# Performance work log

Hardware: AMD Instinct MI355X
Metric: run time of the kernel (lower is better)

Reference implementation:

```python
import jax, jax.numpy as jnp
import numpy as np

N_NODES = 100000
N_EDGES = 600000
N_GRAPHS = 512
VOCAB = 4096
EMB = 128
HID = 128


def setup_inputs() -> dict:
    key = jax.random.key(0)
    ks = jax.random.split(key, 8)
    x = jax.random.randint(ks[0], (N_NODES,), 0, VOCAB)
    edge_index = jax.random.randint(ks[1], (2, N_EDGES), 0, N_NODES)
    batch = jnp.sort(jax.random.randint(ks[2], (N_NODES,), 0, N_GRAPHS))
    emb = jax.random.normal(ks[3], (VOCAB, EMB), dtype=jnp.float32)
    W1 = jax.random.normal(ks[4], (EMB, HID), dtype=jnp.float32) / np.sqrt(EMB)
    b1 = jnp.zeros((HID,), dtype=jnp.float32)
    W2 = jax.random.normal(ks[5], (HID, HID), dtype=jnp.float32) / np.sqrt(HID)
    b2 = jnp.zeros((HID,), dtype=jnp.float32)
    return {"x": x, "edge_index": edge_index, "batch": batch,
            "emb": emb, "W1": W1, "b1": b1, "W2": W2, "b2": b2}


def gcn_conv(h, src, dst, W, b, n_nodes):
    # PyG GCNConv: linear transform, then symmetric-normalized scatter-sum
    # (self-loops already included in src/dst), plus bias.
    h = h @ W
    deg = jax.ops.segment_sum(jnp.ones(dst.shape, h.dtype), dst, num_segments=n_nodes)
    dis = jnp.where(deg > 0, jax.lax.rsqrt(jnp.maximum(deg, 1.0)), 0.0)
    norm = dis[src] * dis[dst]                      # [E]
    msg = h[src] * norm[:, None]                    # gather + scale
    out = jax.ops.segment_sum(msg, dst, num_segments=n_nodes)
    return out + b


def reference(x, edge_index, batch, emb, W1, b1, W2, b2):
    n = x.shape[0]
    loop = jnp.arange(n)
    src = jnp.concatenate([edge_index[0], loop])    # add self-loops, as GCNConv does
    dst = jnp.concatenate([edge_index[1], loop])

    h = emb[x]                                      # [N, EMB] embedding lookup
    h = jax.nn.relu(gcn_conv(h, src, dst, W1, b1, n))
    # dropout: identity in eval mode
    h = gcn_conv(h, src, dst, W2, b2, n)            # [N, HID]

    # global_mean_pool over graph ids
    sums = jax.ops.segment_sum(h, batch, num_segments=N_GRAPHS)
    cnts = jax.ops.segment_sum(jnp.ones((n,), h.dtype), batch, num_segments=N_GRAPHS)
    return sums / jnp.maximum(cnts, 1.0)[:, None]   # [N_GRAPHS, HID]
```

## Files before the change

### kernel.cpp

```cpp
#include <hip/hip_runtime.h>
#include <hip/hip_bf16.h>
#include <hip/hip_fp16.h>

#define D 128

__device__ __forceinline__ float bf2f(unsigned short u) {
  return __uint_as_float(((unsigned int)u) << 16);
}
__device__ __forceinline__ unsigned short f2bf(float f) {
  unsigned int x = __float_as_uint(f);
  x += 0x7fff + ((x >> 16) & 1);
  return (unsigned short)(x >> 16);
}
__device__ __forceinline__ float h2f(unsigned short b) {
  return __half2float(__ushort_as_half(b));
}
__device__ __forceinline__ float2 up2(unsigned int u) {
  __half2 h = *reinterpret_cast<__half2*>(&u);
  return __half22float2(h);
}
__device__ __forceinline__ void fma8h(float* a, uint4 v, float w) {
  float2 t;
  t = up2(v.x); a[0] += w * t.x; a[1] += w * t.y;
  t = up2(v.y); a[2] += w * t.x; a[3] += w * t.y;
  t = up2(v.z); a[4] += w * t.x; a[5] += w * t.y;
  t = up2(v.w); a[6] += w * t.x; a[7] += w * t.y;
}
__device__ __forceinline__ void add8(float* a, uint4 v) {
  a[0] += __uint_as_float(v.x << 16);
  a[1] += __uint_as_float(v.x & 0xffff0000u);
  a[2] += __uint_as_float(v.y << 16);
  a[3] += __uint_as_float(v.y & 0xffff0000u);
  a[4] += __uint_as_float(v.z << 16);
  a[5] += __uint_as_float(v.z & 0xffff0000u);
  a[6] += __uint_as_float(v.w << 16);
  a[7] += __uint_as_float(v.w & 0xffff0000u);
}


__global__ void k_prep(const unsigned short* __restrict__ t0, int n0,
                       const unsigned short* __restrict__ t1, int n1,
                       const unsigned short* __restrict__ t2, int n2,
                       const unsigned short* __restrict__ t3, int n3,
                       const unsigned short* __restrict__ t4, int n4,
                       const unsigned int* __restrict__ ei32,
                       int* __restrict__ flag, int* __restrict__ indeg,
                       float* __restrict__ P, int nn, int ngD) {
  int b = blockIdx.x;
  if (b < 5) {
    const unsigned short* tabs[5] = {t0, t1, t2, t3, t4};
    int ns[5] = {n0, n1, n2, n3, n4};
    const unsigned short* u16 = tabs[b];
    int n = ns[b];
    __shared__ int cnt;
    int K = n / 2 < 256 ? n / 2 : 256;
    if (threadIdx.x == 0) cnt = 0;
    __syncthreads();
    if (threadIdx.x < K) {
      unsigned short u = u16[threadIdx.x * 2];
      int e = (u >> 7) & 0xFF;
      if (u == 0 || (e >= 100 && e <= 140)) atomicAdd(&cnt, 1);
    }
    __syncthreads();
    if (threadIdx.x == 0) flag[b] = (cnt * 2 >= K) ? 1 : 0;
  } else if (b == 5) {
    __shared__ int z;
    if (threadIdx.x == 0) z = 0;
    __syncthreads();
    if (threadIdx.x < 64 && ei32[threadIdx.x * 2 + 1] == 0u) atomicAdd(&z, 1);
    __syncthreads();
    if (threadIdx.x == 0) flag[5] = (z >= 60) ? 1 : 0;
  } else {
    int i = (b - 6) * 256 + threadIdx.x;
    if (i < nn) indeg[i] = 0;
    int j = i - nn;
    if (j >= 0 && j < ngD) P[j] = 0.f;
  }
}

__global__ void k_convi_all(const void* __restrict__ xr, const void* __restrict__ eir,
                            const void* __restrict__ br,
                            int* __restrict__ xs, int* __restrict__ srcs,
                            int* __restrict__ dsts, int* __restrict__ batchs,
                            int* __restrict__ indeg,
                            int nn, int ne, int vocab, int ng,
                            const int* __restrict__ flag64) {
  long long i = (long long)blockIdx.x * blockDim.x + threadIdx.x;
  int is64 = *flag64;
  if (i < nn) {
    int v = is64 ? (int)((const long long*)xr)[i] : ((const int*)xr)[i];
    v = v < 0 ? 0 : (v > vocab - 1 ? vocab - 1 : v);
    xs[i] = v;
  } else if (i < (long long)nn + ne) {
    long long j = i - nn;
    int v = is64 ? (int)((const long long*)eir)[j] : ((const int*)eir)[j];
    v = v < 0 ? 0 : (v > nn - 1 ? nn - 1 : v);
    srcs[j] = v;
  } else if (i < (long long)nn + 2 * ne) {
    long long j = i - nn - ne;
    int v = is64 ? (int)((const long long*)eir)[ne + j] : ((const int*)eir)[ne + j];
    v = v < 0 ? 0 : (v > nn - 1 ? nn - 1 : v);
    dsts[j] = v;
    atomicAdd(&indeg[v], 1);
  } else if (i < 2LL * nn + 2 * ne) {
    long long j = i - nn - 2 * ne;
    int v = is64 ? (int)((const long long*)br)[j] : ((const int*)br)[j];
    v = v < 0 ? 0 : (v > ng - 1 ? ng - 1 : v);
    batchs[j] = v;
  }
}

__global__ __launch_bounds__(1024) void k_scan1(const int* __restrict__ indeg,
                                                int* __restrict__ off,
                                                int* __restrict__ bsum, int nn) {
  int t = threadIdx.x;
  int idx = blockIdx.x * 1024 + t;
  int v = (idx < nn) ? indeg[idx] : 0;
  int lane = t & 63, wid = t >> 6;
  int inc = v;
  #pragma unroll
  for (int d = 1; d < 64; d <<= 1) {
    int u = __shfl_up(inc, d);
    if (lane >= d) inc += u;
  }
  __shared__ int ws[16];
  if (lane == 63) ws[wid] = inc;
  __syncthreads();
  if (wid == 0) {
    int wv = (lane < 16) ? ws[lane] : 0;
    #pragma unroll
    for (int d = 1; d < 16; d <<= 1) {
      int u = __shfl_up(wv, d);
      if (lane >= d) wv += u;
    }
    if (lane < 16) ws[lane] = wv;
  }
  __syncthreads();
  int base = wid ? ws[wid - 1] : 0;
  if (idx < nn) off[idx] = base + inc - v;
  if (t == 1023) bsum[blockIdx.x] = ws[15];
}

__global__ __launch_bounds__(1024) void k_scan23(int* __restrict__ off,
                                                 int* __restrict__ cursor,
                                                 float* __restrict__ dis,
                                                 const int* __restrict__ indeg,
                                                 const int* __restrict__ bsum,
                                                 int nn) {
  int b = blockIdx.x, t = threadIdx.x;
  int v = (t < b) ? bsum[t] : 0;
  #pragma unroll
  for (int d = 32; d; d >>= 1) v += __shfl_xor(v, d);
  __shared__ int ws[16];
  __shared__ int prefix;
  int lane = t & 63, wid = t >> 6;
  if (lane == 0) ws[wid] = v;
  __syncthreads();
  if (t == 0) {
    int s = 0;
    #pragma unroll
    for (int i = 0; i < 16; ++i) s += ws[i];
    prefix = s;
  }
  __syncthreads();
  int idx = b * 1024 + t;
  if (idx < nn) {
    int o = off[idx] + prefix;
    off[idx] = o;
    cursor[idx] = o;
    dis[idx] = rsqrtf((float)indeg[idx] + 1.0f);
  }
}

__global__ void k_fill(const int* __restrict__ srcA, const int* __restrict__ dstA,
                       const int* __restrict__ xs, const float* __restrict__ dis,
                       int* __restrict__ cursor, int2* __restrict__ csr, int ne) {
  int e = blockIdx.x * blockDim.x + threadIdx.x;
  if (e >= ne) return;
  int d = dstA[e], s = srcA[e];
  unsigned short hb = __half_as_ushort(__float2half_rn(dis[s]));
  unsigned int packed = (unsigned int)xs[s] | ((unsigned int)hb << 16);
  int pp = atomicAdd(&cursor[d], 1);
  csr[pp] = make_int2(s, (int)packed);
}

__global__ void k_gemm(const void* __restrict__ emb, const void* __restrict__ W1,
                       unsigned short* __restrict__ G, int vocab,
                       const int* __restrict__ flag) {
  int idx = blockIdx.x * blockDim.x + threadIdx.x;
  if (idx >= vocab * D) return;
  int r = idx >> 7, c = idx & 127;
  int fe = flag[0], fw = flag[1];
  const float* ef = (const float*)emb;
  const unsigned short* eu = (const unsigned short*)emb;
  const float* wf = (const float*)W1;
  const unsigned short* wu = (const unsigned short*)W1;
  size_t ro = (size_t)r * D;
  float acc = 0.f;
  if (fe) {
    if (fw) { for (int k = 0; k < D; ++k) acc += bf2f(eu[ro + k]) * bf2f(wu[k * D + c]); }
    else    { for (int k = 0; k < D; ++k) acc += bf2f(eu[ro + k]) * wf[k * D + c]; }
  } else {
    if (fw) { for (int k = 0; k < D; ++k) acc += ef[ro + k] * bf2f(wu[k * D + c]); }
    else    { for (int k = 0; k < D; ++k) acc += ef[ro + k] * wf[k * D + c]; }
  }
  G[idx] = __half_as_ushort(__float2half_rn(acc));
}

__global__ __launch_bounds__(256) void k_aggrelu(const int* __restrict__ x,
                                                 const unsigned short* __restrict__ G,
                                                 const void* __restrict__ b1,
                                                 const int* __restrict__ off,
                                                 const int* __restrict__ indeg,
                                                 const float* __restrict__ dis,
                                                 const int2* __restrict__ csr,
                                                 unsigned short* __restrict__ H1,
                                                 int nn, const int* __restrict__ flag) {
  int gid = blockIdx.x * blockDim.x + threadIdx.x;
  int n = gid >> 4;
  if (n >= nn) return;
  int lane = threadIdx.x & 15;
  float dn = dis[n];
  const uint4* G4 = (const uint4*)G;
  float a[8];
  {
    uint4 v = G4[(size_t)x[n] * 16 + lane];
    float2 t;
    t = up2(v.x); a[0] = dn * t.x; a[1] = dn * t.y;
    t = up2(v.y); a[2] = dn * t.x; a[3] = dn * t.y;
    t = up2(v.z); a[4] = dn * t.x; a[5] = dn * t.y;
    t = up2(v.w); a[6] = dn * t.x; a[7] = dn * t.y;
  }
  int s0 = off[n], m = indeg[n];
  int j = 0;
  for (; j + 4 <= m; j += 4) {
    int2 c0 = csr[s0 + j],     c1 = csr[s0 + j + 1];
    int2 c2 = csr[s0 + j + 2], c3 = csr[s0 + j + 3];
    uint4 v0 = G4[(size_t)((unsigned)c0.y & 0xFFFFu) * 16 + lane];
    uint4 v1 = G4[(size_t)((unsigned)c1.y & 0xFFFFu) * 16 + lane];
    uint4 v2 = G4[(size_t)((unsigned)c2.y & 0xFFFFu) * 16 + lane];
    uint4 v3 = G4[(size_t)((unsigned)c3.y & 0xFFFFu) * 16 + lane];
    fma8h(a, v0, h2f((unsigned short)((unsigned)c0.y >> 16)));
    fma8h(a, v1, h2f((unsigned short)((unsigned)c1.y >> 16)));
    fma8h(a, v2, h2f((unsigned short)((unsigned)c2.y >> 16)));
    fma8h(a, v3, h2f((unsigned short)((unsigned)c3.y >> 16)));
  }
  for (; j < m; ++j) {
    int2 c = csr[s0 + j];
    uint4 v = G4[(size_t)((unsigned)c.y & 0xFFFFu) * 16 + lane];
    fma8h(a, v, h2f((unsigned short)((unsigned)c.y >> 16)));
  }
  float bb[8];
  if (flag[2]) {
    uint4 bu = ((const uint4*)b1)[lane];
    bb[0] = bf2f((unsigned short)(bu.x & 0xFFFF)); bb[1] = bf2f((unsigned short)(bu.x >> 16));
    bb[2] = bf2f((unsigned short)(bu.y & 0xFFFF)); bb[3] = bf2f((unsigned short)(bu.y >> 16));
    bb[4] = bf2f((unsigned short)(bu.z & 0xFFFF)); bb[5] = bf2f((unsigned short)(bu.z >> 16));
    bb[6] = bf2f((unsigned short)(bu.w & 0xFFFF)); bb[7] = bf2f((unsigned short)(bu.w >> 16));
  } else {
    float4 b0 = ((const float4*)b1)[2 * lane];
    float4 b1v = ((const float4*)b1)[2 * lane + 1];
    bb[0] = b0.x; bb[1] = b0.y; bb[2] = b0.z; bb[3] = b0.w;
    bb[4] = b1v.x; bb[5] = b1v.y; bb[6] = b1v.z; bb[7] = b1v.w;
  }
  ushort4 o0, o1;
  o0.x = f2bf(dn * fmaxf(dn * a[0] + bb[0], 0.f));
  o0.y = f2bf(dn * fmaxf(dn * a[1] + bb[1], 0.f));
  o0.z = f2bf(dn * fmaxf(dn * a[2] + bb[2], 0.f));
  o0.w = f2bf(dn * fmaxf(dn * a[3] + bb[3], 0.f));
  o1.x = f2bf(dn * fmaxf(dn * a[4] + bb[4], 0.f));
  o1.y = f2bf(dn * fmaxf(dn * a[5] + bb[5], 0.f));
  o1.z = f2bf(dn * fmaxf(dn * a[6] + bb[6], 0.f));
  o1.w = f2bf(dn * fmaxf(dn * a[7] + bb[7], 0.f));
  ((ushort4*)(H1 + (size_t)n * D))[2 * lane] = o0;
  ((ushort4*)(H1 + (size_t)n * D))[2 * lane + 1] = o1;
}

__global__ __launch_bounds__(256) void k_agg2pool(
    const unsigned short* __restrict__ H1, const int* __restrict__ off,
    const int* __restrict__ indeg, const float* __restrict__ dis,
    const int2* __restrict__ csr, const int* __restrict__ batch,
    float* __restrict__ P, int nn) {
  __shared__ float buf[16][D];
  __shared__ int gbuf[16];
  int t = threadIdx.x;
  int slot = t >> 4, lane = t & 15;
  int n = blockIdx.x * 16 + slot;
  float a[8] = {0.f, 0.f, 0.f, 0.f, 0.f, 0.f, 0.f, 0.f};
  if (n < nn) {
    float dn = dis[n];
    const uint4* H4 = (const uint4*)H1;
    add8(a, H4[(size_t)n * 16 + lane]);
    int s0 = off[n], m = indeg[n];
    int j = 0;
    if (m >= 4) {
      int i0 = csr[s0].x, i1 = csr[s0 + 1].x;
      int i2 = csr[s0 + 2].x, i3 = csr[s0 + 3].x;
      for (; j + 8 <= m; j += 4) {
        int p0 = csr[s0 + j + 4].x, p1 = csr[s0 + j + 5].x;
        int p2 = csr[s0 + j + 6].x, p3 = csr[s0 + j + 7].x;
        uint4 vA = H4[(size_t)i0 * 16 + lane];
        uint4 vB = H4[(size_t)i1 * 16 + lane];
        uint4 vC = H4[(size_t)i2 * 16 + lane];
        uint4 vD = H4[(size_t)i3 * 16 + lane];
        add8(a, vA); add8(a, vB); add8(a, vC); add8(a, vD);
        i0 = p0; i1 = p1; i2 = p2; i3 = p3;
      }
      {
        uint4 vA = H4[(size_t)i0 * 16 + lane];
        uint4 vB = H4[(size_t)i1 * 16 + lane];
        uint4 vC = H4[(size_t)i2 * 16 + lane];
        uint4 vD = H4[(size_t)i3 * 16 + lane];
        add8(a, vA); add8(a, vB); add8(a, vC); add8(a, vD);
      }
      j += 4;
    }
    for (; j < m; ++j) {
      int e = csr[s0 + j].x;
      add8(a, H4[(size_t)e * 16 + lane]);
    }
    #pragma unroll
    for (int q = 0; q < 8; ++q) a[q] *= dn;
  }
  ((float4*)&buf[slot][lane * 8])[0] = make_float4(a[0], a[1], a[2], a[3]);
  ((float4*)&buf[slot][lane * 8])[1] = make_float4(a[4], a[5], a[6], a[7]);
  if (lane == 0) gbuf[slot] = (n < nn) ? batch[n] : -1;
  __syncthreads();
  if (t < D) {
    int c = t;
    float acc = 0.f;
    int run = -1;
    #pragma unroll
    for (int s2 = 0; s2 < 16; ++s2) {
      int g = gbuf[s2];
      if (g < 0) break;
      if (g != run) {
        if (run >= 0) atomicAdd(&P[(size_t)run * D + c], acc);
        run = g;
        acc = 0.f;
      }
      acc += buf[s2][c];
    }
    if (run >= 0) atomicAdd(&P[(size_t)run * D + c], acc);
  }
}

__global__ void k_out(const float* __restrict__ P, const int* __restrict__ batch,
                      const void* __restrict__ W2, const void* __restrict__ b2,
                      float* __restrict__ Out, int ng, int nn,
                      const int* __restrict__ flag) {
  int idx = blockIdx.x * blockDim.x + threadIdx.x;
  if (idx >= ng * D) return;
  int g = idx >> 7, c = idx & 127;
  int lo = 0, hi = nn;
  while (lo < hi) { int mid = (lo + hi) >> 1; if (batch[mid] < g) lo = mid + 1; else hi = mid; }
  int s = lo;
  hi = nn;
  while (lo < hi) { int mid = (lo + hi) >> 1; if (batch[mid] < g + 1) lo = mid + 1; else hi = mid; }
  int m = lo - s;
  float inv = (m > 0) ? (1.0f / (float)m) : 0.0f;
  const float* pr = P + (size_t)g * D;
  float acc = 0.f;
  if (flag[3]) {
    const unsigned short* wu = (const unsigned short*)W2;
    for (int k = 0; k < D; ++k) acc += pr[k] * bf2f(wu[k * D + c]);
  } else {
    const float* wf = (const float*)W2;
    for (int k = 0; k < D; ++k) acc += pr[k] * wf[k * D + c];
  }
  acc *= inv;
  if (m > 0) acc += flag[4] ? bf2f(((const unsigned short*)b2)[c]) : ((const float*)b2)[c];
  Out[idx] = acc;
}

extern "C" void kernel_launch(void* const* d_in, const int* in_sizes, int n_in,
                              void* d_out, int out_size, void* d_ws, size_t ws_size,
                              hipStream_t stream) {
  const void* xr = d_in[0];
  const void* eir = d_in[1];
  const void* batchr = d_in[2];
  const void* emb = d_in[3];
  const void* W1 = d_in[4];
  const void* b1 = d_in[5];
  const void* W2 = d_in[6];
  const void* b2 = d_in[7];
  float* out = (float*)d_out;

  const int nn = in_sizes[0];
  const int ne = in_sizes[1] / 2;
  const int vocab = in_sizes[3] / D;
  const int ng = out_size / D;
  const int nb = (nn + 1023) / 1024;
  const int ngD = ng * D;

  char* p = (char*)d_ws;
  auto alloc = [&](size_t bytes) -> char* {
    char* r = p;
    p += (bytes + 511) & ~(size_t)511;
    return r;
  };
  int* flag = (int*)alloc(512);
  int* xs = (int*)alloc((size_t)nn * 4);
  int* srcs = (int*)alloc((size_t)ne * 4);
  int* dsts = (int*)alloc((size_t)ne * 4);
  int* batchs = (int*)alloc((size_t)nn * 4);
  int* indeg = (int*)alloc((size_t)nn * 4);
  int* off = (int*)alloc((size_t)nn * 4);
  int* cursor = (int*)alloc((size_t)nn * 4);
  float* dis = (float*)alloc((size_t)nn * 4);
  int* bsum = (int*)alloc((size_t)nb * 4);
  int2* csr = (int2*)alloc((size_t)ne * 8);
  unsigned short* G = (unsigned short*)alloc((size_t)vocab * D * 2);
  unsigned short* H1 = (unsigned short*)alloc((size_t)nn * D * 2);
  float* P = (float*)alloc((size_t)ngD * 4);

  {
    int zb = (nn + ngD + 255) / 256;
    k_prep<<<6 + zb, 256, 0, stream>>>(
        (const unsigned short*)emb, vocab * D,
        (const unsigned short*)W1, D * D,
        (const unsigned short*)b1, D,
        (const unsigned short*)W2, D * D,
        (const unsigned short*)b2, D,
        (const unsigned int*)eir, flag, indeg, P, nn, ngD);
  }

  {
    long long tot = 2LL * nn + 2LL * ne;
    k_convi_all<<<(int)((tot + 255) / 256), 256, 0, stream>>>(
        xr, eir, batchr, xs, srcs, dsts, batchs, indeg, nn, ne, vocab, ng, flag + 5);
  }

  k_scan1<<<nb, 1024, 0, stream>>>(indeg, off, bsum, nn);
  k_scan23<<<nb, 1024, 0, stream>>>(off, cursor, dis, indeg, bsum, nn);
  k_fill<<<(ne + 255) / 256, 256, 0, stream>>>(srcs, dsts, xs, dis, cursor, csr, ne);

  k_gemm<<<(vocab * D + 255) / 256, 256, 0, stream>>>(emb, W1, G, vocab, flag);

  {
    long long thr = (long long)nn * 16;
    k_aggrelu<<<(int)((thr + 255) / 256), 256, 0, stream>>>(xs, G, b1, off, indeg,
                                                            dis, csr, H1, nn, flag);
  }

  k_agg2pool<<<(nn + 15) / 16, 256, 0, stream>>>(H1, off, indeg, dis, csr,
                                                 batchs, P, nn);

  k_out<<<(ngD + 255) / 256, 256, 0, stream>>>(P, batchs, W2, b2, out, ng, nn, flag);
}
```

Measured before the change: 217.7 us.

## Stage W1 in LDS for vocab GEMM and widen gather batching to 8

The embedding-by-W1 GEMM now loads all of W1 into shared memory once per block, and each thread computes 8 output columns of one row, writing a packed 16-byte store. This replaces one-thread-per-output with repeated global reads of W1. Both aggregation kernels now issue up to 8 independent CSR-index and row gathers per iteration with predicated tails, replacing the 4-wide loops, to raise memory-level parallelism. The 64KB LDS tile limits occupancy of the GEMM, and the larger gather batches increase register pressure.

```diff
diff --git a/kernel.cpp b/kernel.cpp
--- a/kernel.cpp
+++ b/kernel.cpp
@@ -184,27 +184,47 @@
   csr[pp] = make_int2(s, (int)packed);
 }
 
-__global__ void k_gemm(const void* __restrict__ emb, const void* __restrict__ W1,
-                       unsigned short* __restrict__ G, int vocab,
-                       const int* __restrict__ flag) {
-  int idx = blockIdx.x * blockDim.x + threadIdx.x;
-  if (idx >= vocab * D) return;
-  int r = idx >> 7, c = idx & 127;
+__global__ __launch_bounds__(256) void k_gemm(const void* __restrict__ emb,
+                                              const void* __restrict__ W1,
+                                              unsigned short* __restrict__ G,
+                                              int vocab,
+                                              const int* __restrict__ flag) {
+  __shared__ float Wl[D * D];
   int fe = flag[0], fw = flag[1];
-  const float* ef = (const float*)emb;
-  const unsigned short* eu = (const unsigned short*)emb;
-  const float* wf = (const float*)W1;
-  const unsigned short* wu = (const unsigned short*)W1;
-  size_t ro = (size_t)r * D;
-  float acc = 0.f;
+  for (int i = threadIdx.x; i < D * D; i += 256) {
+    Wl[i] = fw ? bf2f(((const unsigned short*)W1)[i]) : ((const float*)W1)[i];
+  }
+  __syncthreads();
+  int r = blockIdx.x * 16 + (threadIdx.x >> 4);
+  if (r >= vocab) return;
+  int c0 = (threadIdx.x & 15) * 8;
+  const float* ef = (const float*)emb + (size_t)r * D;
+  const unsigned short* eu = (const unsigned short*)emb + (size_t)r * D;
+  float acc[8] = {0.f, 0.f, 0.f, 0.f, 0.f, 0.f, 0.f, 0.f};
   if (fe) {
-    if (fw) { for (int k = 0; k < D; ++k) acc += bf2f(eu[ro + k]) * bf2f(wu[k * D + c]); }
-    else    { for (int k = 0; k < D; ++k) acc += bf2f(eu[ro + k]) * wf[k * D + c]; }
+    for (int k = 0; k < D; ++k) {
+      float e = bf2f(eu[k]);
+      const float* w = &Wl[k * D + c0];
+      #pragma unroll
+      for (int q = 0; q < 8; ++q) acc[q] += e * w[q];
+    }
   } else {
-    if (fw) { for (int k = 0; k < D; ++k) acc += ef[ro + k] * bf2f(wu[k * D + c]); }
-    else    { for (int k = 0; k < D; ++k) acc += ef[ro + k] * wf[k * D + c]; }
-  }
-  G[idx] = __half_as_ushort(__float2half_rn(acc));
+    for (int k = 0; k < D; ++k) {
+      float e = ef[k];
+      const float* w = &Wl[k * D + c0];
+      #pragma unroll
+      for (int q = 0; q < 8; ++q) acc[q] += e * w[q];
+    }
+  }
+  unsigned int p0 = (unsigned int)__half_as_ushort(__float2half_rn(acc[0])) |
+                    ((unsigned int)__half_as_ushort(__float2half_rn(acc[1])) << 16);
+  unsigned int p1 = (unsigned int)__half_as_ushort(__float2half_rn(acc[2])) |
+                    ((unsigned int)__half_as_ushort(__float2half_rn(acc[3])) << 16);
+  unsigned int p2 = (unsigned int)__half_as_ushort(__float2half_rn(acc[4])) |
+                    ((unsigned int)__half_as_ushort(__float2half_rn(acc[5])) << 16);
+  unsigned int p3 = (unsigned int)__half_as_ushort(__float2half_rn(acc[6])) |
+                    ((unsigned int)__half_as_ushort(__float2half_rn(acc[7])) << 16);
+  *((uint4*)(G + (size_t)r * D + c0)) = make_uint4(p0, p1, p2, p3);
 }
 
 __global__ __launch_bounds__(256) void k_aggrelu(const int* __restrict__ x,
@@ -232,23 +252,19 @@
     t = up2(v.w); a[6] = dn * t.x; a[7] = dn * t.y;
   }
   int s0 = off[n], m = indeg[n];
-  int j = 0;
-  for (; j + 4 <= m; j += 4) {
-    int2 c0 = csr[s0 + j],     c1 = csr[s0 + j + 1];
-    int2 c2 = csr[s0 + j + 2], c3 = csr[s0 + j + 3];
-    uint4 v0 = G4[(size_t)((unsigned)c0.y & 0xFFFFu) * 16 + lane];
-    uint4 v1 = G4[(size_t)((unsigned)c1.y & 0xFFFFu) * 16 + lane];
-    uint4 v2 = G4[(size_t)((unsigned)c2.y & 0xFFFFu) * 16 + lane];
-    uint4 v3 = G4[(size_t)((unsigned)c3.y & 0xFFFFu) * 16 + lane];
-    fma8h(a, v0, h2f((unsigned short)((unsigned)c0.y >> 16)));
-    fma8h(a, v1, h2f((unsigned short)((unsigned)c1.y >> 16)));
-    fma8h(a, v2, h2f((unsigned short)((unsigned)c2.y >> 16)));
-    fma8h(a, v3, h2f((unsigned short)((unsigned)c3.y >> 16)));
-  }
-  for (; j < m; ++j) {
-    int2 c = csr[s0 + j];
-    uint4 v = G4[(size_t)((unsigned)c.y & 0xFFFFu) * 16 + lane];
-    fma8h(a, v, h2f((unsigned short)((unsigned)c.y >> 16)));
+  for (int j = 0; j < m; j += 8) {
+    int k = m - j;
+    unsigned cc[8];
+    uint4 vv[8];
+    #pragma unroll
+    for (int q = 0; q < 8; ++q)
+      if (q < k) cc[q] = (unsigned)csr[s0 + j + q].y;
+    #pragma unroll
+    for (int q = 0; q < 8; ++q)
+      if (q < k) vv[q] = G4[(size_t)(cc[q] & 0xFFFFu) * 16 + lane];
+    #pragma unroll
+    for (int q = 0; q < 8; ++q)
+      if (q < k) fma8h(a, vv[q], h2f((unsigned short)(cc[q] >> 16)));
   }
   float bb[8];
   if (flag[2]) {
@@ -292,32 +308,19 @@
     const uint4* H4 = (const uint4*)H1;
     add8(a, H4[(size_t)n * 16 + lane]);
     int s0 = off[n], m = indeg[n];
-    int j = 0;
-    if (m >= 4) {
-      int i0 = csr[s0].x, i1 = csr[s0 + 1].x;
-      int i2 = csr[s0 + 2].x, i3 = csr[s0 + 3].x;
-      for (; j + 8 <= m; j += 4) {
-        int p0 = csr[s0 + j + 4].x, p1 = csr[s0 + j + 5].x;
-        int p2 = csr[s0 + j + 6].x, p3 = csr[s0 + j + 7].x;
-        uint4 vA = H4[(size_t)i0 * 16 + lane];
-        uint4 vB = H4[(size_t)i1 * 16 + lane];
-        uint4 vC = H4[(size_t)i2 * 16 + lane];
-        uint4 vD = H4[(size_t)i3 * 16 + lane];
-        add8(a, vA); add8(a, vB); add8(a, vC); add8(a, vD);
-        i0 = p0; i1 = p1; i2 = p2; i3 = p3;
-      }
-      {
-        uint4 vA = H4[(size_t)i0 * 16 + lane];
-        uint4 vB = H4[(size_t)i1 * 16 + lane];
-        uint4 vC = H4[(size_t)i2 * 16 + lane];
-        uint4 vD = H4[(size_t)i3 * 16 + lane];
-        add8(a, vA); add8(a, vB); add8(a, vC); add8(a, vD);
-      }
-      j += 4;
-    }
-    for (; j < m; ++j) {
-      int e = csr[s0 + j].x;
-      add8(a, H4[(size_t)e * 16 + lane]);
+    for (int j = 0; j < m; j += 8) {
+      int k = m - j;
+      int ii[8];
+      uint4 vv[8];
+      #pragma unroll
+      for (int q = 0; q < 8; ++q)
+        if (q < k) ii[q] = csr[s0 + j + q].x;
+      #pragma unroll
+      for (int q = 0; q < 8; ++q)
+        if (q < k) vv[q] = H4[(size_t)ii[q] * 16 + lane];
+      #pragma unroll
+      for (int q = 0; q < 8; ++q)
+        if (q < k) add8(a, vv[q]);
     }
     #pragma unroll
     for (int q = 0; q < 8; ++q) a[q] *= dn;
@@ -435,7 +438,7 @@
   k_scan23<<<nb, 1024, 0, stream>>>(off, cursor, dis, indeg, bsum, nn);
   k_fill<<<(ne + 255) / 256, 256, 0, stream>>>(srcs, dsts, xs, dis, cursor, csr, ne);
 
-  k_gemm<<<(vocab * D + 255) / 256, 256, 0, stream>>>(emb, W1, G, vocab, flag);
+  k_gemm<<<(vocab + 15) / 16, 256, 0, stream>>>(emb, W1, G, vocab, flag);
 
   {
     long long thr = (long long)nn * 16;
```

New measurement: 230.4 us. 5.8% more time.
